# Optimization experiments

Hardware: AMD Instinct MI355X
Metric: run time of the kernel (lower is better)

The kernel has to match this reference:

```python
import jax, jax.numpy as jnp
import numpy as np

B, H, M, D, MID, DV = 128, 8, 196, 128, 64, 128


def setup_inputs() -> dict:
    key0 = jax.random.key(0)
    ks = jax.random.split(key0, 12)
    query = jax.random.normal(ks[0], (B, H, D), dtype=jnp.float32)
    key = jax.random.normal(ks[1], (B, H, M, D), dtype=jnp.float32)
    att_mask = jax.random.randint(ks[2], (B, M), 0, 2).astype(jnp.float32)
    att_mask = att_mask.at[:, 0].set(1.0)  # guarantee each row has >=1 valid slot
    value1 = jax.random.normal(ks[3], (B, H, DV), dtype=jnp.float32)
    value2 = jax.random.normal(ks[4], (B, H, M, DV), dtype=jnp.float32)
    W_basic = jax.random.normal(ks[5], (D, MID), dtype=jnp.float32) * 0.05
    b_basic = jnp.zeros((MID,), dtype=jnp.float32)
    W_spatial = jax.random.normal(ks[6], (MID, 1), dtype=jnp.float32) * 0.05
    b_spatial = jnp.zeros((1,), dtype=jnp.float32)
    W_channel = jax.random.normal(ks[7], (MID, DV), dtype=jnp.float32) * 0.05
    b_channel = jnp.zeros((DV,), dtype=jnp.float32)
    return {
        'query': query, 'key': key, 'att_mask': att_mask,
        'value1': value1, 'value2': value2,
        'W_basic': W_basic, 'b_basic': b_basic,
        'W_spatial': W_spatial, 'b_spatial': b_spatial,
        'W_channel': W_channel, 'b_channel': b_channel,
    }


def reference(query, key, att_mask, value1, value2,
              W_basic, b_basic, W_spatial, b_spatial, W_channel, b_channel):
    # att_map: broadcast elementwise QK product  [B,H,M,D]
    att_map = query[..., None, :] * key
    # attention_basic: Linear + ReLU (Dropout is identity at eval)  [B,H,M,MID]
    h = jax.nn.relu(jnp.einsum('bhmd,de->bhme', att_map, W_basic) + b_basic)
    # masked mean-pool over regions  [B,H,MID]
    mask_ext = att_mask[:, None, :, None]  # [B,1,M,1]
    att_map_pool = jnp.sum(h * mask_ext, axis=-2) / jnp.sum(mask_ext, axis=-2)
    # spatial attention logits  [B,H,M]
    alpha_spatial = (jnp.einsum('bhme,eo->bhmo', h, W_spatial) + b_spatial)[..., 0]
    alpha_spatial = jnp.where(att_mask[:, None, :] == 0, -1e9, alpha_spatial)
    alpha_spatial = jax.nn.softmax(alpha_spatial, axis=-1)
    # weighted sum over regions  [B,H,DV]
    v2 = jnp.einsum('bhm,bhmv->bhv', alpha_spatial, value2)
    # channel gate  [B,H,DV]
    alpha_channel = jax.nn.sigmoid(jnp.einsum('bhe,ev->bhv', att_map_pool, W_channel) + b_channel)
    return value1 * v2 * alpha_channel
```

## Files before the change

kernel.cpp:

```cpp
#include <hip/hip_runtime.h>
#include <cstddef>

#define NBH  1024
#define Mm   196
#define Dd   128
#define MIDe 64
#define DVv  128
#define WQLD 136

typedef __attribute__((ext_vector_type(8))) short bf16x8;
typedef __attribute__((ext_vector_type(4))) float f32x4;

__device__ __forceinline__ short f2bf(float x) {
    union { float f; unsigned u; } v; v.f = x;
    return (short)((v.u + 0x7FFFu + ((v.u >> 16) & 1u)) >> 16);
}

__device__ __forceinline__ float waveReduceSum(float v) {
#pragma unroll
    for (int off = 32; off > 0; off >>= 1) v += __shfl_xor(v, off, 64);
    return v;
}

__global__ __launch_bounds__(256, 4)
void scatt_fused(const float* __restrict__ query,
                 const float* __restrict__ key,
                 const float* __restrict__ att_mask,
                 const float* __restrict__ value1,
                 const float* __restrict__ value2,
                 const float* __restrict__ W_basic,
                 const float* __restrict__ b_basic,
                 const float* __restrict__ W_spatial,
                 const float* __restrict__ b_spatial,
                 const float* __restrict__ W_channel,
                 const float* __restrict__ b_channel,
                 float* __restrict__ out)
{
    __shared__ short wqT[MIDe][WQLD];
    __shared__ float qS[Dd];
    __shared__ float maskS[Mm];
    __shared__ float poolPart[4][MIDe];
    __shared__ float poolS[MIDe];
    __shared__ float accW[4][DVv];
    __shared__ float mW[4], lW[4], cntW[4];

    const int t    = threadIdx.x;
    const int lane = t & 63;
    const int w    = t >> 6;
    const int ln15 = lane & 15;
    const int q4   = lane >> 4;
    const int bh   = blockIdx.x;
    const int b    = bh >> 3;

    const float* __restrict__ keyB  = key      + (size_t)bh * Mm * Dd;
    const float* __restrict__ val2B = value2   + (size_t)bh * Mm * DVv;
    const float* __restrict__ qB    = query    + (size_t)bh * Dd;
    const float* __restrict__ maskB = att_mask + (size_t)b  * Mm;

    if (t < 32) ((float4*)qS)[t] = ((const float4*)qB)[t];
    for (int i = t; i < Mm; i += 256) maskS[i] = maskB[i];
    __syncthreads();

    {
        const int e0 = lane;
        const int d0 = w * 32;
#pragma unroll
        for (int c = 0; c < 4; ++c) {
            short pk[8];
#pragma unroll
            for (int j = 0; j < 8; ++j) {
                const int d = d0 + c * 8 + j;
                pk[j] = f2bf(qS[d] * W_basic[d * MIDe + e0]);
            }
            *(bf16x8*)&wqT[e0][d0 + c * 8] = *(bf16x8*)pk;
        }
    }
    __syncthreads();

    float bbv[4], wspv[4];
#pragma unroll
    for (int nt = 0; nt < 4; ++nt) {
        bbv[nt]  = b_basic[nt * 16 + ln15];
        wspv[nt] = W_spatial[nt * 16 + ln15];
    }
    const float bsp = b_spatial[0];

    float poolAcc[4] = {0.f, 0.f, 0.f, 0.f};
    float m_run = -3.0e38f;
    float l_run = 0.f;
    float2 av   = make_float2(0.f, 0.f);

    for (int mt = w; mt < 13; mt += 4) {
        const int mrow = min(mt * 16 + ln15, Mm - 1);
        const float* ap = keyB + (size_t)mrow * Dd + q4 * 8;
        float4 a0[4], a1[4];
#pragma unroll
        for (int ks = 0; ks < 4; ++ks) {
            a0[ks] = *(const float4*)(ap + ks * 32);
            a1[ks] = *(const float4*)(ap + ks * 32 + 4);
        }
        float2 vv[16];
        {
            const float* vp = val2B + 2 * lane;
#pragma unroll
            for (int i = 0; i < 16; ++i) {
                const int mc = min(mt * 16 + i, Mm - 1);
                vv[i] = *(const float2*)(vp + (size_t)mc * DVv);
            }
        }

        f32x4 acc[4] = {f32x4{0,0,0,0}, f32x4{0,0,0,0},
                        f32x4{0,0,0,0}, f32x4{0,0,0,0}};
#pragma unroll
        for (int ks = 0; ks < 4; ++ks) {
            const bf16x8 af = { f2bf(a0[ks].x), f2bf(a0[ks].y),
                                f2bf(a0[ks].z), f2bf(a0[ks].w),
                                f2bf(a1[ks].x), f2bf(a1[ks].y),
                                f2bf(a1[ks].z), f2bf(a1[ks].w) };
#pragma unroll
            for (int nt = 0; nt < 4; ++nt) {
                const bf16x8 bk =
                    *(const bf16x8*)&wqT[nt * 16 + ln15][ks * 32 + q4 * 8];
                acc[nt] = __builtin_amdgcn_mfma_f32_16x16x32_bf16(
                              af, bk, acc[nt], 0, 0, 0);
            }
        }

        float sR[4];
#pragma unroll
        for (int r = 0; r < 4; ++r) {
            const int m = mt * 16 + q4 * 4 + r;
            const bool valid = m < Mm;
            const float msk = valid ? maskS[m] : 0.f;
            float srow = 0.f;
#pragma unroll
            for (int nt = 0; nt < 4; ++nt) {
                float hv = acc[nt][r] + bbv[nt];
                hv = hv > 0.f ? hv : 0.f;
                poolAcc[nt] = fmaf(hv, msk, poolAcc[nt]);
                srow = fmaf(hv, wspv[nt], srow);
            }
            srow += __shfl_xor(srow, 1, 64);
            srow += __shfl_xor(srow, 2, 64);
            srow += __shfl_xor(srow, 4, 64);
            srow += __shfl_xor(srow, 8, 64);
            sR[r] = valid ? (msk == 0.f ? -1.0e9f : srow + bsp) : -3.0e38f;
        }

        float sv[16];
#pragma unroll
        for (int i = 0; i < 16; ++i)
            sv[i] = __shfl(sR[i & 3], (i >> 2) << 4, 64);

        float tm = sv[0];
#pragma unroll
        for (int i = 1; i < 16; ++i) tm = fmaxf(tm, sv[i]);

        const float newm = fmaxf(m_run, tm);
        const float sc = __expf(m_run - newm);
        m_run = newm;
        l_run *= sc;
        av.x *= sc; av.y *= sc;
#pragma unroll
        for (int i = 0; i < 16; ++i) {
            const float p = __expf(sv[i] - newm);
            l_run += p;
            av.x = fmaf(p, vv[i].x, av.x);
            av.y = fmaf(p, vv[i].y, av.y);
        }
    }

#pragma unroll
    for (int nt = 0; nt < 4; ++nt) {
        poolAcc[nt] += __shfl_xor(poolAcc[nt], 16, 64);
        poolAcc[nt] += __shfl_xor(poolAcc[nt], 32, 64);
    }
    if (lane < 16) {
#pragma unroll
        for (int nt = 0; nt < 4; ++nt)
            poolPart[w][nt * 16 + lane] = poolAcc[nt];
    }
    {
        const int mi = w * 64 + lane;
        float cm = (mi < Mm) ? maskS[mi] : 0.f;
        cm = waveReduceSum(cm);
        if (lane == 0) cntW[w] = cm;
    }
    if (lane == 0) { mW[w] = m_run; lW[w] = l_run; }
    ((float2*)&accW[w][0])[lane] = av;
    __syncthreads();

    float v2v = 0.f;
    if (t < DVv) {
        const float M = fmaxf(fmaxf(mW[0], mW[1]), fmaxf(mW[2], mW[3]));
        float L = 0.f;
#pragma unroll
        for (int i = 0; i < 4; ++i) {
            const float s = __expf(mW[i] - M);
            L   = fmaf(lW[i], s, L);
            v2v = fmaf(accW[i][t], s, v2v);
        }
        v2v /= L;
    }
    if (t < MIDe) {
        const float cnt = cntW[0] + cntW[1] + cntW[2] + cntW[3];
        poolS[t] = (poolPart[0][t] + poolPart[1][t] +
                    poolPart[2][t] + poolPart[3][t]) / cnt;
    }
    __syncthreads();

    if (t < DVv) {
        float a = b_channel[t];
#pragma unroll 8
        for (int e = 0; e < MIDe; ++e)
            a = fmaf(poolS[e], W_channel[e * DVv + t], a);
        const float chv = 1.f / (1.f + __expf(-a));
        out[(size_t)bh * DVv + t] = value1[(size_t)bh * DVv + t] * v2v * chv;
    }
}

extern "C" void kernel_launch(void* const* d_in, const int* in_sizes, int n_in,
                              void* d_out, int out_size, void* d_ws, size_t ws_size,
                              hipStream_t stream) {
    const float* query     = (const float*)d_in[0];
    const float* key       = (const float*)d_in[1];
    const float* att_mask  = (const float*)d_in[2];
    const float* value1    = (const float*)d_in[3];
    const float* value2    = (const float*)d_in[4];
    const float* W_basic   = (const float*)d_in[5];
    const float* b_basic   = (const float*)d_in[6];
    const float* W_spatial = (const float*)d_in[7];
    const float* b_spatial = (const float*)d_in[8];
    const float* W_channel = (const float*)d_in[9];
    const float* b_channel = (const float*)d_in[10];
    float* out = (float*)d_out;

    scatt_fused<<<NBH, 256, 0, stream>>>(query, key, att_mask, value1, value2,
                                         W_basic, b_basic, W_spatial, b_spatial,
                                         W_channel, b_channel, out);
}
```

Before: 268.1 us.

## Process two m-tiles per iteration to raise memory-level parallelism in fused attention

Restructures the per-wave loop over m-tiles into two unrolled rounds that each load and compute two 16-row tiles (A and B), so key and value2 loads for both tiles are in flight together. Exponentials are computed once per row and then broadcast instead of broadcasting logits, and the online softmax rescale is merged across both tiles with split accumulators. Launch bounds drop to 2 blocks per SM to give the larger register footprint room, at the cost of lower occupancy. Tile A is assumed always valid, so its bounds checks are dropped, and the tail tile handles the partial last rows explicitly.

```diff
diff --git a/kernel.cpp b/kernel.cpp
--- a/kernel.cpp
+++ b/kernel.cpp
@@ -22,7 +22,7 @@
     return v;
 }
 
-__global__ __launch_bounds__(256, 4)
+__global__ __launch_bounds__(256, 2)
 void scatt_fused(const float* __restrict__ query,
                  const float* __restrict__ key,
                  const float* __restrict__ att_mask,
@@ -90,52 +90,113 @@
     float l_run = 0.f;
     float2 av   = make_float2(0.f, 0.f);
 
-    for (int mt = w; mt < 13; mt += 4) {
-        const int mrow = min(mt * 16 + ln15, Mm - 1);
-        const float* ap = keyB + (size_t)mrow * Dd + q4 * 8;
-        float4 a0[4], a1[4];
+#pragma unroll
+    for (int r = 0; r < 2; ++r) {
+        const int mtA = w + r * 8;
+        const int mtB = mtA + 4;
+        const bool hasB = (mtB < 13);
+
+        const int mrowA = min(mtA * 16 + ln15, Mm - 1);
+        const float* apA = keyB + (size_t)mrowA * Dd + q4 * 8;
+        float4 a0A[4], a1A[4];
 #pragma unroll
         for (int ks = 0; ks < 4; ++ks) {
-            a0[ks] = *(const float4*)(ap + ks * 32);
-            a1[ks] = *(const float4*)(ap + ks * 32 + 4);
-        }
-        float2 vv[16];
+            a0A[ks] = *(const float4*)(apA + ks * 32);
+            a1A[ks] = *(const float4*)(apA + ks * 32 + 4);
+        }
+        float4 a0B[4], a1B[4];
         {
-            const float* vp = val2B + 2 * lane;
-#pragma unroll
-            for (int i = 0; i < 16; ++i) {
-                const int mc = min(mt * 16 + i, Mm - 1);
-                vv[i] = *(const float2*)(vp + (size_t)mc * DVv);
-            }
-        }
-
-        f32x4 acc[4] = {f32x4{0,0,0,0}, f32x4{0,0,0,0},
-                        f32x4{0,0,0,0}, f32x4{0,0,0,0}};
+            const int mrowB = min(mtB * 16 + ln15, Mm - 1);
+            const float* apB = keyB + (size_t)mrowB * Dd + q4 * 8;
+            if (hasB) {
+#pragma unroll
+                for (int ks = 0; ks < 4; ++ks) {
+                    a0B[ks] = *(const float4*)(apB + ks * 32);
+                    a1B[ks] = *(const float4*)(apB + ks * 32 + 4);
+                }
+            }
+        }
+
+        const float* vpA0 = val2B + (size_t)(mtA * 16) * DVv + 2 * lane;
+        const float* vpA1 = vpA0 + 8 * DVv;
+        float2 vvA[16];
+#pragma unroll
+        for (int i = 0; i < 8; ++i) vvA[i]     = *(const float2*)(vpA0 + i * DVv);
+#pragma unroll
+        for (int i = 0; i < 8; ++i) vvA[8 + i] = *(const float2*)(vpA1 + i * DVv);
+
+        float2 vvB[16];
+        {
+            const float* vpB0 = val2B + (size_t)(mtB * 16) * DVv + 2 * lane;
+            const float* vpB1 = vpB0 + 8 * DVv;
+            if (hasB) {
+                if (mtB < 12) {
+#pragma unroll
+                    for (int i = 0; i < 8; ++i) vvB[i]     = *(const float2*)(vpB0 + i * DVv);
+#pragma unroll
+                    for (int i = 0; i < 8; ++i) vvB[8 + i] = *(const float2*)(vpB1 + i * DVv);
+                } else {
+#pragma unroll
+                    for (int i = 0; i < 4; ++i) vvB[i] = *(const float2*)(vpB0 + i * DVv);
+#pragma unroll
+                    for (int i = 4; i < 8; ++i) vvB[i] = make_float2(0.f, 0.f);
+#pragma unroll
+                    for (int i = 0; i < 8; ++i) vvB[8 + i] = make_float2(0.f, 0.f);
+                }
+            }
+        }
+
+        bf16x8 afA[4];
+#pragma unroll
+        for (int ks = 0; ks < 4; ++ks)
+            afA[ks] = bf16x8{ f2bf(a0A[ks].x), f2bf(a0A[ks].y),
+                              f2bf(a0A[ks].z), f2bf(a0A[ks].w),
+                              f2bf(a1A[ks].x), f2bf(a1A[ks].y),
+                              f2bf(a1A[ks].z), f2bf(a1A[ks].w) };
+        f32x4 accA[4] = {f32x4{0,0,0,0}, f32x4{0,0,0,0},
+                         f32x4{0,0,0,0}, f32x4{0,0,0,0}};
 #pragma unroll
         for (int ks = 0; ks < 4; ++ks) {
-            const bf16x8 af = { f2bf(a0[ks].x), f2bf(a0[ks].y),
-                                f2bf(a0[ks].z), f2bf(a0[ks].w),
-                                f2bf(a1[ks].x), f2bf(a1[ks].y),
-                                f2bf(a1[ks].z), f2bf(a1[ks].w) };
 #pragma unroll
             for (int nt = 0; nt < 4; ++nt) {
                 const bf16x8 bk =
                     *(const bf16x8*)&wqT[nt * 16 + ln15][ks * 32 + q4 * 8];
-                acc[nt] = __builtin_amdgcn_mfma_f32_16x16x32_bf16(
-                              af, bk, acc[nt], 0, 0, 0);
-            }
-        }
-
-        float sR[4];
-#pragma unroll
-        for (int r = 0; r < 4; ++r) {
-            const int m = mt * 16 + q4 * 4 + r;
-            const bool valid = m < Mm;
-            const float msk = valid ? maskS[m] : 0.f;
+                accA[nt] = __builtin_amdgcn_mfma_f32_16x16x32_bf16(
+                               afA[ks], bk, accA[nt], 0, 0, 0);
+            }
+        }
+
+        bf16x8 afB[4];
+        f32x4 accB[4] = {f32x4{0,0,0,0}, f32x4{0,0,0,0},
+                         f32x4{0,0,0,0}, f32x4{0,0,0,0}};
+        if (hasB) {
+#pragma unroll
+            for (int ks = 0; ks < 4; ++ks)
+                afB[ks] = bf16x8{ f2bf(a0B[ks].x), f2bf(a0B[ks].y),
+                                  f2bf(a0B[ks].z), f2bf(a0B[ks].w),
+                                  f2bf(a1B[ks].x), f2bf(a1B[ks].y),
+                                  f2bf(a1B[ks].z), f2bf(a1B[ks].w) };
+#pragma unroll
+            for (int ks = 0; ks < 4; ++ks) {
+#pragma unroll
+                for (int nt = 0; nt < 4; ++nt) {
+                    const bf16x8 bk =
+                        *(const bf16x8*)&wqT[nt * 16 + ln15][ks * 32 + q4 * 8];
+                    accB[nt] = __builtin_amdgcn_mfma_f32_16x16x32_bf16(
+                                   afB[ks], bk, accB[nt], 0, 0, 0);
+                }
+            }
+        }
+
+        float sRA[4], sRB[4];
+#pragma unroll
+        for (int rr = 0; rr < 4; ++rr) {
+            const int m = mtA * 16 + q4 * 4 + rr;
+            const float msk = maskS[m];
             float srow = 0.f;
 #pragma unroll
             for (int nt = 0; nt < 4; ++nt) {
-                float hv = acc[nt][r] + bbv[nt];
+                float hv = accA[nt][rr] + bbv[nt];
                 hv = hv > 0.f ? hv : 0.f;
                 poolAcc[nt] = fmaf(hv, msk, poolAcc[nt]);
                 srow = fmaf(hv, wspv[nt], srow);
@@ -144,30 +205,82 @@
             srow += __shfl_xor(srow, 2, 64);
             srow += __shfl_xor(srow, 4, 64);
             srow += __shfl_xor(srow, 8, 64);
-            sR[r] = valid ? (msk == 0.f ? -1.0e9f : srow + bsp) : -3.0e38f;
-        }
-
-        float sv[16];
-#pragma unroll
-        for (int i = 0; i < 16; ++i)
-            sv[i] = __shfl(sR[i & 3], (i >> 2) << 4, 64);
-
-        float tm = sv[0];
-#pragma unroll
-        for (int i = 1; i < 16; ++i) tm = fmaxf(tm, sv[i]);
-
+            sRA[rr] = (msk == 0.f) ? -1.0e9f : srow + bsp;
+        }
+        float tmA = fmaxf(fmaxf(sRA[0], sRA[1]), fmaxf(sRA[2], sRA[3]));
+        tmA = fmaxf(tmA, __shfl_xor(tmA, 16, 64));
+        tmA = fmaxf(tmA, __shfl_xor(tmA, 32, 64));
+
+        float tmB = -3.0e38f;
+        if (hasB) {
+#pragma unroll
+            for (int rr = 0; rr < 4; ++rr) {
+                const int m = mtB * 16 + q4 * 4 + rr;
+                const bool valid = m < Mm;
+                const float msk = valid ? maskS[m] : 0.f;
+                float srow = 0.f;
+#pragma unroll
+                for (int nt = 0; nt < 4; ++nt) {
+                    float hv = accB[nt][rr] + bbv[nt];
+                    hv = hv > 0.f ? hv : 0.f;
+                    poolAcc[nt] = fmaf(hv, msk, poolAcc[nt]);
+                    srow = fmaf(hv, wspv[nt], srow);
+                }
+                srow += __shfl_xor(srow, 1, 64);
+                srow += __shfl_xor(srow, 2, 64);
+                srow += __shfl_xor(srow, 4, 64);
+                srow += __shfl_xor(srow, 8, 64);
+                sRB[rr] = valid ? (msk == 0.f ? -1.0e9f : srow + bsp) : -3.0e38f;
+            }
+            tmB = fmaxf(fmaxf(sRB[0], sRB[1]), fmaxf(sRB[2], sRB[3]));
+            tmB = fmaxf(tmB, __shfl_xor(tmB, 16, 64));
+            tmB = fmaxf(tmB, __shfl_xor(tmB, 32, 64));
+        }
+
+        const float tm   = hasB ? fmaxf(tmA, tmB) : tmA;
         const float newm = fmaxf(m_run, tm);
-        const float sc = __expf(m_run - newm);
+        const float sc   = __expf(m_run - newm);
         m_run = newm;
-        l_run *= sc;
-        av.x *= sc; av.y *= sc;
-#pragma unroll
-        for (int i = 0; i < 16; ++i) {
-            const float p = __expf(sv[i] - newm);
-            l_run += p;
-            av.x = fmaf(p, vv[i].x, av.x);
-            av.y = fmaf(p, vv[i].y, av.y);
-        }
+
+        float lsum = 0.f;
+        float ax0 = 0.f, ax1 = 0.f, ay0 = 0.f, ay1 = 0.f;
+        {
+            float p4[4];
+#pragma unroll
+            for (int rr = 0; rr < 4; ++rr) p4[rr] = __expf(sRA[rr] - newm);
+            float pv[16];
+#pragma unroll
+            for (int i = 0; i < 16; ++i)
+                pv[i] = __shfl(p4[i & 3], (i >> 2) << 4, 64);
+#pragma unroll
+            for (int i = 0; i < 16; i += 2) {
+                lsum += pv[i] + pv[i + 1];
+                ax0 = fmaf(pv[i],     vvA[i].x,     ax0);
+                ay0 = fmaf(pv[i],     vvA[i].y,     ay0);
+                ax1 = fmaf(pv[i + 1], vvA[i + 1].x, ax1);
+                ay1 = fmaf(pv[i + 1], vvA[i + 1].y, ay1);
+            }
+        }
+        if (hasB) {
+            float p4[4];
+#pragma unroll
+            for (int rr = 0; rr < 4; ++rr) p4[rr] = __expf(sRB[rr] - newm);
+            float pv[16];
+#pragma unroll
+            for (int i = 0; i < 16; ++i)
+                pv[i] = __shfl(p4[i & 3], (i >> 2) << 4, 64);
+#pragma unroll
+            for (int i = 0; i < 16; i += 2) {
+                lsum += pv[i] + pv[i + 1];
+                ax0 = fmaf(pv[i],     vvB[i].x,     ax0);
+                ay0 = fmaf(pv[i],     vvB[i].y,     ay0);
+                ax1 = fmaf(pv[i + 1], vvB[i + 1].x, ax1);
+                ay1 = fmaf(pv[i + 1], vvB[i + 1].y, ay1);
+            }
+        }
+        l_run = fmaf(l_run, sc, lsum);
+        av.x  = fmaf(av.x,  sc, ax0 + ax1);
+        av.y  = fmaf(av.y,  sc, ay0 + ay1);
     }
 
 #pragma unroll
```

Measured after the change: 243.2 us. 9.3% less time.

## Double-buffer key tiles into LDS via async loads and split DV across waves

Applied to the files above, without the earlier changes.

Key rows are now streamed into a double-buffered LDS tile with global_load_lds. All four waves process every 16-row M tile together, with the next tile's load issued before computing the current one. Each wave now owns a 32-column slice of DV instead of a slice of M, so the cross-wave softmax merge and pool reduction become in-wave shuffles. This removes one block barrier and the LDS partial buffers. In exchange there is a block barrier per tile, hand-placed waitcnt and sched_barrier constraints, and a fully unrolled 13-step loop that raises code size and register pressure.

```diff
diff --git a/kernel.cpp b/kernel.cpp
--- a/kernel.cpp
+++ b/kernel.cpp
@@ -16,10 +16,10 @@
     return (short)((v.u + 0x7FFFu + ((v.u >> 16) & 1u)) >> 16);
 }
 
-__device__ __forceinline__ float waveReduceSum(float v) {
-#pragma unroll
-    for (int off = 32; off > 0; off >>= 1) v += __shfl_xor(v, off, 64);
-    return v;
+__device__ __forceinline__ void gl_lds16(const void* g, void* l) {
+    __builtin_amdgcn_global_load_lds(
+        (const __attribute__((address_space(1))) unsigned int*)g,
+        (__attribute__((address_space(3))) unsigned int*)l, 16, 0, 0);
 }
 
 __global__ __launch_bounds__(256, 4)
@@ -36,13 +36,11 @@
                  const float* __restrict__ b_channel,
                  float* __restrict__ out)
 {
-    __shared__ short wqT[MIDe][WQLD];
-    __shared__ float qS[Dd];
-    __shared__ float maskS[Mm];
-    __shared__ float poolPart[4][MIDe];
-    __shared__ float poolS[MIDe];
-    __shared__ float accW[4][DVv];
-    __shared__ float mW[4], lW[4], cntW[4];
+    __shared__ float4 kb[2][32][16];
+    __shared__ short  wqT[MIDe][WQLD];
+    __shared__ float  qS[Dd];
+    __shared__ float  maskS[Mm];
+    __shared__ float  poolS[MIDe];
 
     const int t    = threadIdx.x;
     const int lane = t & 63;
@@ -52,15 +50,31 @@
     const int bh   = blockIdx.x;
     const int b    = bh >> 3;
 
-    const float* __restrict__ keyB  = key      + (size_t)bh * Mm * Dd;
-    const float* __restrict__ val2B = value2   + (size_t)bh * Mm * DVv;
-    const float* __restrict__ qB    = query    + (size_t)bh * Dd;
-    const float* __restrict__ maskB = att_mask + (size_t)b  * Mm;
+    const char*  keyC  = (const char*)(key + (size_t)bh * Mm * Dd);
+    const float* val2B = value2   + (size_t)bh * Mm * DVv;
+    const float* qB    = query    + (size_t)bh * Dd;
+    const float* maskB = att_mask + (size_t)b  * Mm;
+
+    int so[2], soT[2];
+#pragma unroll
+    for (int j = 0; j < 2; ++j) {
+        const int cell = w * 128 + j * 64 + lane;
+        const int d4 = cell >> 4, row = cell & 15;
+        so[j]  = row * 512 + d4 * 16;
+        soT[j] = (row < 4 ? row : 3) * 512 + d4 * 16;
+    }
+    const int colOff = w * 32 + 2 * ln15;
+
+    gl_lds16(keyC + so[0], (char*)kb + w * 2048);
+    gl_lds16(keyC + so[1], (char*)kb + w * 2048 + 1024);
+    float2 vv[2][4];
+#pragma unroll
+    for (int rr = 0; rr < 4; ++rr)
+        vv[0][rr] = *(const float2*)(val2B + (size_t)(q4 * 4 + rr) * DVv + colOff);
 
     if (t < 32) ((float4*)qS)[t] = ((const float4*)qB)[t];
     for (int i = t; i < Mm; i += 256) maskS[i] = maskB[i];
     __syncthreads();
-
     {
         const int e0 = lane;
         const int d0 = w * 32;
@@ -86,37 +100,44 @@
     const float bsp = b_spatial[0];
 
     float poolAcc[4] = {0.f, 0.f, 0.f, 0.f};
-    float m_run = -3.0e38f;
-    float l_run = 0.f;
-    float2 av   = make_float2(0.f, 0.f);
-
-    for (int mt = w; mt < 13; mt += 4) {
-        const int mrow = min(mt * 16 + ln15, Mm - 1);
-        const float* ap = keyB + (size_t)mrow * Dd + q4 * 8;
-        float4 a0[4], a1[4];
-#pragma unroll
-        for (int ks = 0; ks < 4; ++ks) {
-            a0[ks] = *(const float4*)(ap + ks * 32);
-            a1[ks] = *(const float4*)(ap + ks * 32 + 4);
-        }
-        float2 vv[16];
-        {
-            const float* vp = val2B + 2 * lane;
-#pragma unroll
-            for (int i = 0; i < 16; ++i) {
-                const int mc = min(mt * 16 + i, Mm - 1);
-                vv[i] = *(const float2*)(vp + (size_t)mc * DVv);
-            }
-        }
-
+    float m_run = -3.0e38f, l_run = 0.f;
+    float2 av = make_float2(0.f, 0.f);
+
+#pragma unroll
+    for (int mt = 0; mt < 13; ++mt) {
+        asm volatile("s_waitcnt vmcnt(4)" ::: "memory");
+        __builtin_amdgcn_s_barrier();
+        __builtin_amdgcn_sched_barrier(0);
+        if (mt < 12) {
+            char* db = (char*)kb + ((mt + 1) & 1) * 8192;
+            const char* sb = keyC + (size_t)(mt + 1) * 8192;
+            if (mt + 1 < 12) {
+                gl_lds16(sb + so[0], db + w * 2048);
+                gl_lds16(sb + so[1], db + w * 2048 + 1024);
+            } else {
+                gl_lds16(sb + soT[0], db + w * 2048);
+                gl_lds16(sb + soT[1], db + w * 2048 + 1024);
+            }
+            __builtin_amdgcn_sched_barrier(0);
+#pragma unroll
+            for (int rr = 0; rr < 4; ++rr) {
+                int vrow = (mt + 1) * 16 + q4 * 4 + rr;
+                if (mt + 1 == 12) vrow = vrow < Mm ? vrow : (Mm - 1);
+                vv[(mt + 1) & 1][rr] =
+                    *(const float2*)(val2B + (size_t)vrow * DVv + colOff);
+            }
+        }
+
+        const char* kbB = (const char*)kb + (mt & 1) * 8192;
         f32x4 acc[4] = {f32x4{0,0,0,0}, f32x4{0,0,0,0},
                         f32x4{0,0,0,0}, f32x4{0,0,0,0}};
 #pragma unroll
         for (int ks = 0; ks < 4; ++ks) {
-            const bf16x8 af = { f2bf(a0[ks].x), f2bf(a0[ks].y),
-                                f2bf(a0[ks].z), f2bf(a0[ks].w),
-                                f2bf(a1[ks].x), f2bf(a1[ks].y),
-                                f2bf(a1[ks].z), f2bf(a1[ks].w) };
+            const int d4 = ks * 8 + q4 * 2;
+            const float4 f0 = *(const float4*)(kbB + d4 * 256 + ln15 * 16);
+            const float4 f1 = *(const float4*)(kbB + d4 * 256 + 256 + ln15 * 16);
+            const bf16x8 af = { f2bf(f0.x), f2bf(f0.y), f2bf(f0.z), f2bf(f0.w),
+                                f2bf(f1.x), f2bf(f1.y), f2bf(f1.z), f2bf(f1.w) };
 #pragma unroll
             for (int nt = 0; nt < 4; ++nt) {
                 const bf16x8 bk =
@@ -128,14 +149,14 @@
 
         float sR[4];
 #pragma unroll
-        for (int r = 0; r < 4; ++r) {
-            const int m = mt * 16 + q4 * 4 + r;
-            const bool valid = m < Mm;
-            const float msk = valid ? maskS[m] : 0.f;
+        for (int rr = 0; rr < 4; ++rr) {
+            const int m = mt * 16 + q4 * 4 + rr;
+            const bool valid = (mt < 12) || (m < Mm);
+            const float msk = valid ? maskS[m < Mm ? m : (Mm - 1)] : 0.f;
             float srow = 0.f;
 #pragma unroll
             for (int nt = 0; nt < 4; ++nt) {
-                float hv = acc[nt][r] + bbv[nt];
+                float hv = acc[nt][rr] + bbv[nt];
                 hv = hv > 0.f ? hv : 0.f;
                 poolAcc[nt] = fmaf(hv, msk, poolAcc[nt]);
                 srow = fmaf(hv, wspv[nt], srow);
@@ -144,29 +165,22 @@
             srow += __shfl_xor(srow, 2, 64);
             srow += __shfl_xor(srow, 4, 64);
             srow += __shfl_xor(srow, 8, 64);
-            sR[r] = valid ? (msk == 0.f ? -1.0e9f : srow + bsp) : -3.0e38f;
-        }
-
-        float sv[16];
-#pragma unroll
-        for (int i = 0; i < 16; ++i)
-            sv[i] = __shfl(sR[i & 3], (i >> 2) << 4, 64);
-
-        float tm = sv[0];
-#pragma unroll
-        for (int i = 1; i < 16; ++i) tm = fmaxf(tm, sv[i]);
+            sR[rr] = valid ? (msk == 0.f ? -1.0e9f : srow + bsp) : -3.0e38f;
+        }
+        float tm = fmaxf(fmaxf(sR[0], sR[1]), fmaxf(sR[2], sR[3]));
+        tm = fmaxf(tm, __shfl_xor(tm, 16, 64));
+        tm = fmaxf(tm, __shfl_xor(tm, 32, 64));
 
         const float newm = fmaxf(m_run, tm);
         const float sc = __expf(m_run - newm);
         m_run = newm;
-        l_run *= sc;
-        av.x *= sc; av.y *= sc;
-#pragma unroll
-        for (int i = 0; i < 16; ++i) {
-            const float p = __expf(sv[i] - newm);
+        l_run *= sc; av.x *= sc; av.y *= sc;
+#pragma unroll
+        for (int rr = 0; rr < 4; ++rr) {
+            const float p = __expf(sR[rr] - newm);
             l_run += p;
-            av.x = fmaf(p, vv[i].x, av.x);
-            av.y = fmaf(p, vv[i].y, av.y);
+            av.x = fmaf(p, vv[mt & 1][rr].x, av.x);
+            av.y = fmaf(p, vv[mt & 1][rr].y, av.y);
         }
     }
 
@@ -175,47 +189,49 @@
         poolAcc[nt] += __shfl_xor(poolAcc[nt], 16, 64);
         poolAcc[nt] += __shfl_xor(poolAcc[nt], 32, 64);
     }
-    if (lane < 16) {
+    l_run += __shfl_xor(l_run, 16, 64);
+    l_run += __shfl_xor(l_run, 32, 64);
+    av.x  += __shfl_xor(av.x, 16, 64);
+    av.x  += __shfl_xor(av.x, 32, 64);
+    av.y  += __shfl_xor(av.y, 16, 64);
+    av.y  += __shfl_xor(av.y, 32, 64);
+
+    float cnt = 0.f;
+    for (int i = lane; i < Mm; i += 64) cnt += maskS[i];
+#pragma unroll
+    for (int off = 32; off > 0; off >>= 1) cnt += __shfl_xor(cnt, off, 64);
+
+    if (w == 0 && lane < 16) {
 #pragma unroll
         for (int nt = 0; nt < 4; ++nt)
-            poolPart[w][nt * 16 + lane] = poolAcc[nt];
-    }
-    {
-        const int mi = w * 64 + lane;
-        float cm = (mi < Mm) ? maskS[mi] : 0.f;
-        cm = waveReduceSum(cm);
-        if (lane == 0) cntW[w] = cm;
-    }
-    if (lane == 0) { mW[w] = m_run; lW[w] = l_run; }
-    ((float2*)&accW[w][0])[lane] = av;
+            poolS[nt * 16 + lane] = poolAcc[nt] / cnt;
+    }
     __syncthreads();
 
-    float v2v = 0.f;
-    if (t < DVv) {
-        const float M = fmaxf(fmaxf(mW[0], mW[1]), fmaxf(mW[2], mW[3]));
-        float L = 0.f;
-#pragma unroll
-        for (int i = 0; i < 4; ++i) {
-            const float s = __expf(mW[i] - M);
-            L   = fmaf(lW[i], s, L);
-            v2v = fmaf(accW[i][t], s, v2v);
-        }
-        v2v /= L;
-    }
-    if (t < MIDe) {
-        const float cnt = cntW[0] + cntW[1] + cntW[2] + cntW[3];
-        poolS[t] = (poolPart[0][t] + poolPart[1][t] +
-                    poolPart[2][t] + poolPart[3][t]) / cnt;
-    }
-    __syncthreads();
-
-    if (t < DVv) {
-        float a = b_channel[t];
-#pragma unroll 8
-        for (int e = 0; e < MIDe; ++e)
-            a = fmaf(poolS[e], W_channel[e * DVv + t], a);
-        const float chv = 1.f / (1.f + __expf(-a));
-        out[(size_t)bh * DVv + t] = value1[(size_t)bh * DVv + t] * v2v * chv;
+    const float v2x = av.x / l_run;
+    const float v2y = av.y / l_run;
+
+    float a0 = 0.f, a1 = 0.f;
+#pragma unroll
+    for (int i = 0; i < 16; ++i) {
+        const int e = q4 * 16 + i;
+        const float pe = poolS[e];
+        const float2 wc = *(const float2*)(W_channel + (size_t)e * DVv + colOff);
+        a0 = fmaf(pe, wc.x, a0);
+        a1 = fmaf(pe, wc.y, a1);
+    }
+    a0 += __shfl_xor(a0, 16, 64); a0 += __shfl_xor(a0, 32, 64);
+    a1 += __shfl_xor(a1, 16, 64); a1 += __shfl_xor(a1, 32, 64);
+
+    if (q4 == 0) {
+        const float2 bc = *(const float2*)(b_channel + colOff);
+        const float ch0 = 1.f / (1.f + __expf(-(a0 + bc.x)));
+        const float ch1 = 1.f / (1.f + __expf(-(a1 + bc.y)));
+        const float2 v1 = *(const float2*)(value1 + (size_t)bh * DVv + colOff);
+        float2 o;
+        o.x = v1.x * v2x * ch0;
+        o.y = v1.y * v2y * ch1;
+        *(float2*)(out + (size_t)bh * DVv + colOff) = o;
     }
 }
 
```

Measured after the change: 441.0 us. 1.64x slower.
